# Kernel tuning notes

Hardware: AMD Instinct MI355X
Metric: run time of the kernel (lower is better)

Reference implementation:

```python
import jax, jax.numpy as jnp
import numpy as np

DIM = 1024      # dim
FW = 14         # focal_window
FL = 2          # focal_level
FF = 4          # focal_factor


def _dwconv_gelu(x, w, b):
    # x: [B, C, S], w: [C, 1, k] depthwise kernel, torch 'same' padding
    k = w.shape[-1]
    y = jax.lax.conv_general_dilated(
        x, w, window_strides=(1,), padding=[((k - 1) // 2, k // 2)],
        feature_group_count=x.shape[1], dimension_numbers=('NCH', 'OIH', 'NCH'))
    return jax.nn.gelu(y + b[None, :, None], approximate=False)


def setup_inputs() -> dict:
    key = jax.random.key(0)
    ks = jax.random.split(key, 8)
    B, S, D = 8, 4096, DIM
    P = 2 * D + FL + 1  # 2051
    s = 0.02
    return {
        'input': jax.random.normal(ks[0], (B, S, D), jnp.float32),
        'W_in': jax.random.normal(ks[1], (D, P), jnp.float32) * s,
        'b_in': jnp.zeros((P,), jnp.float32),
        'w0': jax.random.normal(ks[2], (D, 1, FW), jnp.float32) * s,
        'b0': jnp.zeros((D,), jnp.float32),
        'w1': jax.random.normal(ks[3], (D, 1, FF + FW), jnp.float32) * s,  # kernel 18
        'b1': jnp.zeros((D,), jnp.float32),
        'W_ctx': jax.random.normal(ks[4], (D, D), jnp.float32) * s,
        'b_ctx': jnp.zeros((D,), jnp.float32),
        'W_out': jax.random.normal(ks[5], (D, D), jnp.float32) * s,
        'b_out': jnp.zeros((D,), jnp.float32),
    }


def reference(input, W_in, b_in, w0, b0, w1, b1, W_ctx, b_ctx, W_out, b_out):
    D = DIM
    # in_proj then permute to channel-first [B, 2D+FL+1, S]
    proj = (input @ W_in + b_in).transpose(0, 2, 1)
    query = proj[:, :D]            # [B, D, S]
    ctx = proj[:, D:2 * D]         # [B, D, S]
    gates = proj[:, 2 * D:]        # [B, FL+1, S]
    # hierarchical depthwise conv pyramid (context fed through successive levels)
    c0 = _dwconv_gelu(ctx, w0, b0)
    c1 = _dwconv_gelu(c0, w1, b1)
    context_all = c0 * gates[:, 0:1] + c1 * gates[:, 1:2]
    # global context branch
    g = jax.nn.gelu(c1.mean(axis=-1), approximate=False)  # [B, D]
    context_all = context_all + g[..., None] * gates[:, FL:FL + 1]
    # context_proj is a 1x1 conv == per-position linear over channels
    modulator = jnp.einsum('oc,bcs->bos', W_ctx, context_all) + b_ctx[None, :, None]
    out = (query * modulator).transpose(0, 2, 1)  # [B, S, D]
    return out @ W_out + b_out
```

## Files before the change

### kernel.cpp

```cpp
#include <hip/hip_runtime.h>

#define DIMC 1024
#define BATCH 8
#define SEQ 4096
#define BS (BATCH*SEQ)
#define PCOL 2051

typedef unsigned short ushort_t;
typedef __attribute__((ext_vector_type(8))) short short8;
typedef __attribute__((ext_vector_type(4))) float f32x4;
typedef __attribute__((ext_vector_type(4))) unsigned short us4;

__device__ __forceinline__ float bf2f(ushort_t u) {
    union { unsigned u32; float f; } v; v.u32 = ((unsigned)u) << 16; return v.f;
}
__device__ __forceinline__ ushort_t f2bf(float f) {
    union { float f; unsigned u; } v; v.f = f;
    unsigned r = v.u + 0x7fffu + ((v.u >> 16) & 1u);
    return (ushort_t)(r >> 16);
}
__device__ __forceinline__ float gelu_exact(float x) {
    return 0.5f * x * (1.0f + erff(x * 0.7071067811865475f));
}
__device__ __forceinline__ void gld16(const ushort_t* g, ushort_t* l) {
    __builtin_amdgcn_global_load_lds(
        (const __attribute__((address_space(1))) unsigned int*)g,
        (__attribute__((address_space(3))) unsigned int*)l, 16, 0, 0);
}

__global__ void cvt_f32_bf16(const float* __restrict__ src, ushort_t* __restrict__ dst, int n) {
    int i = (blockIdx.x * 256 + threadIdx.x) * 4;
    if (i >= n) return;
    f32x4 v = *(const f32x4*)(src + i);
    us4 o;
    #pragma unroll
    for (int j = 0; j < 4; j++) o[j] = f2bf(v[j]);
    *(us4*)(dst + i) = o;
}

__global__ void transpose_cvt(const float* __restrict__ src, ushort_t* __restrict__ dst,
                              int ld, int K) {
    __shared__ float tile[32][33];
    int tx = threadIdx.x & 31, ty = threadIdx.x >> 5;
    int n0 = blockIdx.x * 32, k0 = blockIdx.y * 32;
    #pragma unroll
    for (int j = 0; j < 4; j++)
        tile[ty + j * 8][tx] = src[(size_t)(k0 + ty + j * 8) * ld + n0 + tx];
    __syncthreads();
    #pragma unroll
    for (int j = 0; j < 4; j++)
        dst[(size_t)(n0 + ty + j * 8) * K + k0 + tx] = f2bf(tile[tx][ty + j * 8]);
}

__global__ void pack_gatesw(const float* __restrict__ W_in, float* __restrict__ wg) {
    int d = blockIdx.x * 256 + threadIdx.x;
    if (d >= 1024) return;
    const float* p = W_in + (size_t)d * PCOL + 2048;
    wg[d] = p[0]; wg[1024 + d] = p[1]; wg[2048 + d] = p[2];
}

__global__ void cvt_gates(const float* __restrict__ input, const float* __restrict__ wg,
                          const float* __restrict__ b_in, ushort_t* __restrict__ ibf,
                          float* __restrict__ gates) {
    int row = blockIdx.x, tid = threadIdx.x;
    int lane = tid & 63, wave = tid >> 6;
    size_t base = (size_t)row * 1024 + tid * 4;
    f32x4 v = *(const f32x4*)(input + base);
    us4 o;
    #pragma unroll
    for (int j = 0; j < 4; j++) o[j] = f2bf(v[j]);
    *(us4*)(ibf + base) = o;
    f32x4 w0v = *(const f32x4*)(wg + tid * 4);
    f32x4 w1v = *(const f32x4*)(wg + 1024 + tid * 4);
    f32x4 w2v = *(const f32x4*)(wg + 2048 + tid * 4);
    float a0 = 0, a1 = 0, a2 = 0;
    #pragma unroll
    for (int j = 0; j < 4; j++) { a0 += v[j] * w0v[j]; a1 += v[j] * w1v[j]; a2 += v[j] * w2v[j]; }
    #pragma unroll
    for (int off = 32; off; off >>= 1) {
        a0 += __shfl_down(a0, off, 64);
        a1 += __shfl_down(a1, off, 64);
        a2 += __shfl_down(a2, off, 64);
    }
    __shared__ float red[4][3];
    if (lane == 0) { red[wave][0] = a0; red[wave][1] = a1; red[wave][2] = a2; }
    __syncthreads();
    if (tid == 0) {
        gates[row * 4 + 0] = red[0][0] + red[1][0] + red[2][0] + red[3][0] + b_in[2048];
        gates[row * 4 + 1] = red[0][1] + red[1][1] + red[2][1] + red[3][1] + b_in[2049];
        gates[row * 4 + 2] = red[0][2] + red[1][2] + red[2][2] + red[3][2] + b_in[2050];
    }
}

template<int FUSEQ, int F32OUT>
__global__ __launch_bounds__(256, 2)
void gemm_bt(const ushort_t* __restrict__ A, const ushort_t* __restrict__ Bt,
             const float* __restrict__ bias, void* __restrict__ C,
             const ushort_t* __restrict__ Q, int K, int ldc, int ldq) {
    __shared__ ushort_t lA[128 * 32];
    __shared__ ushort_t lB[128 * 32];
    const int tid = threadIdx.x, lane = tid & 63, wave = tid >> 6;
    const int bn = blockIdx.x, bm = blockIdx.y;
    const int wm = (wave >> 1) * 64, wn = (wave & 1) * 64;
    const int lr = lane & 15, kq = (lane >> 4) * 8;

    const ushort_t* Ag = A + (size_t)bm * 128 * K;
    const ushort_t* Bg = Bt + (size_t)bn * 128 * K;

    f32x4 acc[4][4];
    #pragma unroll
    for (int i = 0; i < 4; i++)
        #pragma unroll
        for (int j = 0; j < 4; j++)
            #pragma unroll
            for (int r = 0; r < 4; r++) acc[i][j][r] = 0.0f;

    for (int k0 = 0; k0 < K; k0 += 32) {
        #pragma unroll
        for (int i = 0; i < 2; i++) {
            int cb = i * 256 + wave * 64;
            int c  = cb + lane;
            int row = c >> 2, kk = (c & 3) << 3;
            gld16(Ag + (size_t)row * K + kk, &lA[cb << 3]);
            gld16(Bg + (size_t)row * K + kk, &lB[cb << 3]);
        }
        Ag += 32; Bg += 32;
        __syncthreads();

        short8 af[4], bfr[4];
        #pragma unroll
        for (int mt = 0; mt < 4; mt++)
            af[mt] = *(const short8*)&lA[(wm + mt * 16 + lr) * 32 + kq];
        #pragma unroll
        for (int nt = 0; nt < 4; nt++)
            bfr[nt] = *(const short8*)&lB[(wn + nt * 16 + lr) * 32 + kq];
        #pragma unroll
        for (int mt = 0; mt < 4; mt++)
            #pragma unroll
            for (int nt = 0; nt < 4; nt++)
                acc[mt][nt] = __builtin_amdgcn_mfma_f32_16x16x32_bf16(
                    af[mt], bfr[nt], acc[mt][nt], 0, 0, 0);
        __syncthreads();
    }

    const int lq = lane >> 4;
    #pragma unroll
    for (int mt = 0; mt < 4; mt++) {
        #pragma unroll
        for (int r = 0; r < 4; r++) {
            int row = bm * 128 + wm + mt * 16 + lq * 4 + r;
            size_t rowc = (size_t)row * ldc;
            #pragma unroll
            for (int nt = 0; nt < 4; nt++) {
                int col = bn * 128 + wn + nt * 16 + lr;
                float v = acc[mt][nt][r] + bias[col];
                if (FUSEQ) v *= bf2f(Q[(size_t)row * ldq + col]);
                if (F32OUT) ((float*)C)[rowc + col] = v;
                else        ((ushort_t*)C)[rowc + col] = f2bf(v);
            }
        }
    }
}

template<int KW, int PADL, int DOMEAN>
__global__ __launch_bounds__(256)
void dwconv_gelu2(const ushort_t* __restrict__ X, int ldx, int x0,
                  const float* __restrict__ W, const float* __restrict__ Bv,
                  ushort_t* __restrict__ Y, float* __restrict__ G) {
    const int R = 64 + KW - 1;
    __shared__ float xs[(64 + KW - 1) * 64];
    int tid = threadIdx.x;
    int s0 = blockIdx.x * 64, d0 = blockIdx.y * 64, b = blockIdx.z;
    for (int c = tid; c < R * 8; c += 256) {
        int r = c >> 3, dd = (c & 7) * 8;
        int s = s0 + r - PADL;
        float f[8];
        if (s >= 0 && s < SEQ) {
            short8 u = *(const short8*)&X[(size_t)(b * SEQ + s) * ldx + x0 + d0 + dd];
            #pragma unroll
            for (int j = 0; j < 8; j++) f[j] = bf2f((ushort_t)u[j]);
        } else {
            #pragma unroll
            for (int j = 0; j < 8; j++) f[j] = 0.f;
        }
        f32x4 v0 = {f[0], f[1], f[2], f[3]}, v1 = {f[4], f[5], f[6], f[7]};
        *(f32x4*)&xs[r * 64 + dd] = v0;
        *(f32x4*)&xs[r * 64 + dd + 4] = v1;
    }
    int d = tid & 63, sc = tid >> 6;
    float wr[KW];
    #pragma unroll
    for (int t = 0; t < KW; t++) wr[t] = W[(size_t)(d0 + d) * KW + t];
    float bb = Bv[d0 + d];
    __syncthreads();
    float xw[16 + KW - 1];
    #pragma unroll
    for (int r = 0; r < 16 + KW - 1; r++) xw[r] = xs[(sc * 16 + r) * 64 + d];
    float psum = 0.f;
    #pragma unroll
    for (int i = 0; i < 16; i++) {
        float acc = bb;
        #pragma unroll
        for (int t = 0; t < KW; t++) acc += wr[t] * xw[i + t];
        float gv = gelu_exact(acc);
        if (DOMEAN) psum += gv;
        Y[(size_t)(b * SEQ + s0 + sc * 16 + i) * 1024 + d0 + d] = f2bf(gv);
    }
    if (DOMEAN) {
        __shared__ float rs[256];
        rs[tid] = psum;
        __syncthreads();
        if (sc == 0)
            atomicAdd(&G[b * 1024 + d0 + d], rs[d] + rs[64 + d] + rs[128 + d] + rs[192 + d]);
    }
}

__global__ void gelu_g(const float* __restrict__ G, float* __restrict__ gG) {
    int i = blockIdx.x * 256 + threadIdx.x;
    if (i < BATCH * 1024) gG[i] = gelu_exact(G[i] * (1.0f / (float)SEQ));
}

__global__ void combine2(const ushort_t* __restrict__ C0, const ushort_t* __restrict__ C1,
                         const float* __restrict__ gates, const float* __restrict__ gG,
                         ushort_t* __restrict__ CA) {
    int row = blockIdx.x * 2 + (threadIdx.x >> 7);
    int c = (threadIdx.x & 127) * 8;
    int b = row >> 12;
    float g0 = gates[row * 4 + 0], g1 = gates[row * 4 + 1], g2 = gates[row * 4 + 2];
    size_t base = (size_t)row * 1024 + c;
    short8 u0 = *(const short8*)&C0[base];
    short8 u1 = *(const short8*)&C1[base];
    f32x4 gv0 = *(const f32x4*)&gG[b * 1024 + c];
    f32x4 gv1 = *(const f32x4*)&gG[b * 1024 + c + 4];
    short8 o;
    #pragma unroll
    for (int j = 0; j < 8; j++) {
        float gg = (j < 4) ? gv0[j] : gv1[j - 4];
        float v = bf2f((ushort_t)u0[j]) * g0 + bf2f((ushort_t)u1[j]) * g1 + gg * g2;
        o[j] = (short)f2bf(v);
    }
    *(short8*)&CA[base] = o;
}

extern "C" void kernel_launch(void* const* d_in, const int* in_sizes, int n_in,
                              void* d_out, int out_size, void* d_ws, size_t ws_size,
                              hipStream_t stream) {
    const float* input = (const float*)d_in[0];
    const float* W_in  = (const float*)d_in[1];
    const float* b_in  = (const float*)d_in[2];
    const float* w0    = (const float*)d_in[3];
    const float* b0    = (const float*)d_in[4];
    const float* w1    = (const float*)d_in[5];
    const float* b1    = (const float*)d_in[6];
    const float* W_ctx = (const float*)d_in[7];
    const float* b_ctx = (const float*)d_in[8];
    const float* W_out = (const float*)d_in[9];
    const float* b_out = (const float*)d_in[10];

    char* ws = (char*)d_ws;
    size_t o = 0;
    ushort_t* ibf   = (ushort_t*)(ws + o); o += (size_t)BS * 1024 * 2;
    ushort_t* proj  = (ushort_t*)(ws + o); o += (size_t)BS * 2048 * 2;
    ushort_t* c0    = (ushort_t*)(ws + o); o += (size_t)BS * 1024 * 2;
    ushort_t* c1    = (ushort_t*)(ws + o); o += (size_t)BS * 1024 * 2;
    float*    gates = (float*)   (ws + o); o += (size_t)BS * 4 * 4;
    float*    G     = (float*)   (ws + o); o += (size_t)BATCH * 1024 * 4;
    float*    gG    = (float*)   (ws + o); o += (size_t)BATCH * 1024 * 4;
    float*    wg    = (float*)   (ws + o); o += (size_t)3 * 1024 * 4;
    ushort_t* winT  = (ushort_t*)(ws + o); o += (size_t)2048 * 1024 * 2;
    ushort_t* wctxB = (ushort_t*)(ws + o); o += (size_t)1024 * 1024 * 2;
    ushort_t* woutT = (ushort_t*)(ws + o); o += (size_t)1024 * 1024 * 2;
    ushort_t* ca = ibf;
    ushort_t* Y  = c0;

    hipMemsetAsync(G, 0, BATCH * 1024 * sizeof(float), stream);
    pack_gatesw<<<4, 256, 0, stream>>>(W_in, wg);
    transpose_cvt<<<dim3(2048 / 32, 1024 / 32), 256, 0, stream>>>(W_in, winT, PCOL, 1024);
    cvt_f32_bf16<<<1024 * 1024 / 4 / 256, 256, 0, stream>>>(W_ctx, wctxB, 1024 * 1024);
    transpose_cvt<<<dim3(1024 / 32, 1024 / 32), 256, 0, stream>>>(W_out, woutT, 1024, 1024);
    cvt_gates<<<BS, 256, 0, stream>>>(input, wg, b_in, ibf, gates);
    gemm_bt<0, 0><<<dim3(16, 256), 256, 0, stream>>>(ibf, winT, b_in, proj, nullptr, 1024, 2048, 0);
    dwconv_gelu2<14, 6, 0><<<dim3(SEQ / 64, 16, BATCH), 256, 0, stream>>>(proj, 2048, 1024, w0, b0, c0, nullptr);
    dwconv_gelu2<18, 8, 1><<<dim3(SEQ / 64, 16, BATCH), 256, 0, stream>>>(c0, 1024, 0, w1, b1, c1, G);
    gelu_g<<<BATCH * 1024 / 256, 256, 0, stream>>>(G, gG);
    combine2<<<BS / 2, 256, 0, stream>>>(c0, c1, gates, gG, ca);
    gemm_bt<1, 0><<<dim3(8, 256), 256, 0, stream>>>(ca, wctxB, b_ctx, Y, proj, 1024, 1024, 2048);
    gemm_bt<0, 1><<<dim3(8, 256), 256, 0, stream>>>(Y, woutT, b_out, d_out, nullptr, 1024, 1024, 0);
}
```

Baseline: 760.5 us.

## Fuse both depthwise convs with gating and fold global context into GEMM epilogue

```diff
diff --git a/kernel.cpp b/kernel.cpp
--- a/kernel.cpp
+++ b/kernel.cpp
@@ -92,11 +92,12 @@
     }
 }
 
-template<int FUSEQ, int F32OUT>
+template<int MODE>
 __global__ __launch_bounds__(256, 2)
 void gemm_bt(const ushort_t* __restrict__ A, const ushort_t* __restrict__ Bt,
              const float* __restrict__ bias, void* __restrict__ C,
-             const ushort_t* __restrict__ Q, int K, int ldc, int ldq) {
+             const ushort_t* __restrict__ Q, const float* __restrict__ gates,
+             const float* __restrict__ vb, int K, int ldc, int ldq) {
     __shared__ ushort_t lA[128 * 32];
     __shared__ ushort_t lB[128 * 32];
     const int tid = threadIdx.x, lane = tid & 63, wave = tid >> 6;
@@ -144,39 +145,48 @@
     }
 
     const int lq = lane >> 4;
+    const int bbatch = (bm * 128) >> 12;
     #pragma unroll
     for (int mt = 0; mt < 4; mt++) {
         #pragma unroll
         for (int r = 0; r < 4; r++) {
             int row = bm * 128 + wm + mt * 16 + lq * 4 + r;
             size_t rowc = (size_t)row * ldc;
+            float g2;
+            if (MODE == 1) g2 = gates[row * 4 + 2];
             #pragma unroll
             for (int nt = 0; nt < 4; nt++) {
                 int col = bn * 128 + wn + nt * 16 + lr;
                 float v = acc[mt][nt][r] + bias[col];
-                if (FUSEQ) v *= bf2f(Q[(size_t)row * ldq + col]);
-                if (F32OUT) ((float*)C)[rowc + col] = v;
-                else        ((ushort_t*)C)[rowc + col] = f2bf(v);
+                if (MODE == 1) {
+                    v += g2 * vb[bbatch * 1024 + col];
+                    v *= bf2f(Q[(size_t)row * ldq + col]);
+                }
+                if (MODE == 2) ((float*)C)[rowc + col] = v;
+                else           ((ushort_t*)C)[rowc + col] = f2bf(v);
             }
         }
     }
 }
 
-template<int KW, int PADL, int DOMEAN>
 __global__ __launch_bounds__(256)
-void dwconv_gelu2(const ushort_t* __restrict__ X, int ldx, int x0,
-                  const float* __restrict__ W, const float* __restrict__ Bv,
-                  ushort_t* __restrict__ Y, float* __restrict__ G) {
-    const int R = 64 + KW - 1;
-    __shared__ float xs[(64 + KW - 1) * 64];
-    int tid = threadIdx.x;
-    int s0 = blockIdx.x * 64, d0 = blockIdx.y * 64, b = blockIdx.z;
-    for (int c = tid; c < R * 8; c += 256) {
+void dwconv_fused(const ushort_t* __restrict__ proj,
+                  const float* __restrict__ w0, const float* __restrict__ b0,
+                  const float* __restrict__ w1, const float* __restrict__ b1,
+                  const float* __restrict__ gates,
+                  ushort_t* __restrict__ P, float* __restrict__ G) {
+    __shared__ float xc[94 * 64];
+    __shared__ float x0[81 * 64];
+    __shared__ float gl[2][64];
+    __shared__ float rs[256];
+    const int tid = threadIdx.x;
+    const int s0 = blockIdx.x * 64, d0 = blockIdx.y * 64, b = blockIdx.z;
+    for (int c = tid; c < 94 * 8; c += 256) {
         int r = c >> 3, dd = (c & 7) * 8;
-        int s = s0 + r - PADL;
+        int s = s0 - 14 + r;
         float f[8];
         if (s >= 0 && s < SEQ) {
-            short8 u = *(const short8*)&X[(size_t)(b * SEQ + s) * ldx + x0 + d0 + dd];
+            short8 u = *(const short8*)&proj[(size_t)(b * SEQ + s) * 2048 + 1024 + d0 + dd];
             #pragma unroll
             for (int j = 0; j < 8; j++) f[j] = bf2f((ushort_t)u[j]);
         } else {
@@ -184,62 +194,76 @@
             for (int j = 0; j < 8; j++) f[j] = 0.f;
         }
         f32x4 v0 = {f[0], f[1], f[2], f[3]}, v1 = {f[4], f[5], f[6], f[7]};
-        *(f32x4*)&xs[r * 64 + dd] = v0;
-        *(f32x4*)&xs[r * 64 + dd + 4] = v1;
-    }
-    int d = tid & 63, sc = tid >> 6;
-    float wr[KW];
-    #pragma unroll
-    for (int t = 0; t < KW; t++) wr[t] = W[(size_t)(d0 + d) * KW + t];
-    float bb = Bv[d0 + d];
-    __syncthreads();
-    float xw[16 + KW - 1];
-    #pragma unroll
-    for (int r = 0; r < 16 + KW - 1; r++) xw[r] = xs[(sc * 16 + r) * 64 + d];
+        *(f32x4*)&xc[r * 64 + dd] = v0;
+        *(f32x4*)&xc[r * 64 + dd + 4] = v1;
+    }
+    if (tid < 64) gl[0][tid] = gates[(size_t)(b * SEQ + s0 + tid) * 4 + 0];
+    else if (tid < 128) gl[1][tid - 64] = gates[(size_t)(b * SEQ + s0 + tid - 64) * 4 + 1];
+    const int d = tid & 63, sc = tid >> 6;
+    float wr0[14], wr1[18];
+    #pragma unroll
+    for (int t = 0; t < 14; t++) wr0[t] = w0[(size_t)(d0 + d) * 14 + t];
+    float bb0 = b0[d0 + d];
+    #pragma unroll
+    for (int t = 0; t < 18; t++) wr1[t] = w1[(size_t)(d0 + d) * 18 + t];
+    float bb1 = b1[d0 + d];
+    __syncthreads();
+    {
+        float xw[34];
+        int r0 = sc * 20;
+        #pragma unroll
+        for (int r = 0; r < 34; r++) xw[r] = xc[(r0 + r) * 64 + d];
+        #pragma unroll
+        for (int i = 0; i < 21; i++) {
+            int rr = r0 + i;
+            int s = s0 - 8 + rr;
+            float acc = bb0;
+            #pragma unroll
+            for (int t = 0; t < 14; t++) acc += wr0[t] * xw[i + t];
+            x0[rr * 64 + d] = (s >= 0 && s < SEQ) ? gelu_exact(acc) : 0.f;
+        }
+    }
+    __syncthreads();
+    float xw1[33];
+    #pragma unroll
+    for (int r = 0; r < 33; r++) xw1[r] = x0[(sc * 16 + r) * 64 + d];
     float psum = 0.f;
     #pragma unroll
     for (int i = 0; i < 16; i++) {
-        float acc = bb;
-        #pragma unroll
-        for (int t = 0; t < KW; t++) acc += wr[t] * xw[i + t];
-        float gv = gelu_exact(acc);
-        if (DOMEAN) psum += gv;
-        Y[(size_t)(b * SEQ + s0 + sc * 16 + i) * 1024 + d0 + d] = f2bf(gv);
-    }
-    if (DOMEAN) {
-        __shared__ float rs[256];
-        rs[tid] = psum;
-        __syncthreads();
-        if (sc == 0)
-            atomicAdd(&G[b * 1024 + d0 + d], rs[d] + rs[64 + d] + rs[128 + d] + rs[192 + d]);
-    }
-}
-
-__global__ void gelu_g(const float* __restrict__ G, float* __restrict__ gG) {
-    int i = blockIdx.x * 256 + threadIdx.x;
-    if (i < BATCH * 1024) gG[i] = gelu_exact(G[i] * (1.0f / (float)SEQ));
-}
-
-__global__ void combine2(const ushort_t* __restrict__ C0, const ushort_t* __restrict__ C1,
-                         const float* __restrict__ gates, const float* __restrict__ gG,
-                         ushort_t* __restrict__ CA) {
-    int row = blockIdx.x * 2 + (threadIdx.x >> 7);
-    int c = (threadIdx.x & 127) * 8;
-    int b = row >> 12;
-    float g0 = gates[row * 4 + 0], g1 = gates[row * 4 + 1], g2 = gates[row * 4 + 2];
-    size_t base = (size_t)row * 1024 + c;
-    short8 u0 = *(const short8*)&C0[base];
-    short8 u1 = *(const short8*)&C1[base];
-    f32x4 gv0 = *(const f32x4*)&gG[b * 1024 + c];
-    f32x4 gv1 = *(const f32x4*)&gG[b * 1024 + c + 4];
-    short8 o;
-    #pragma unroll
-    for (int j = 0; j < 8; j++) {
-        float gg = (j < 4) ? gv0[j] : gv1[j - 4];
-        float v = bf2f((ushort_t)u0[j]) * g0 + bf2f((ushort_t)u1[j]) * g1 + gg * g2;
-        o[j] = (short)f2bf(v);
-    }
-    *(short8*)&CA[base] = o;
+        float acc = bb1;
+        #pragma unroll
+        for (int t = 0; t < 18; t++) acc += wr1[t] * xw1[i + t];
+        float c1 = gelu_exact(acc);
+        psum += c1;
+        float c0v = xw1[i + 8];
+        int sl = sc * 16 + i;
+        float pv = c0v * gl[0][sl] + c1 * gl[1][sl];
+        P[(size_t)(b * SEQ + s0 + sl) * 1024 + d0 + d] = f2bf(pv);
+    }
+    rs[tid] = psum;
+    __syncthreads();
+    if (sc == 0)
+        atomicAdd(&G[b * 1024 + d0 + d], rs[d] + rs[64 + d] + rs[128 + d] + rs[192 + d]);
+}
+
+__global__ __launch_bounds__(256)
+void gemv_v(const float* __restrict__ G, const ushort_t* __restrict__ wctxB,
+            float* __restrict__ v) {
+    __shared__ float gg[1024];
+    const int tid = threadIdx.x, b = blockIdx.y;
+    for (int i = tid; i < 1024; i += 256)
+        gg[i] = gelu_exact(G[b * 1024 + i] * (1.0f / (float)SEQ));
+    __syncthreads();
+    const int w = tid >> 6, lane = tid & 63;
+    const int o = blockIdx.x * 4 + w;
+    const ushort_t* wr = wctxB + (size_t)o * 1024;
+    float acc = 0.f;
+    #pragma unroll
+    for (int j = 0; j < 16; j++)
+        acc += gg[j * 64 + lane] * bf2f(wr[j * 64 + lane]);
+    #pragma unroll
+    for (int off = 32; off; off >>= 1) acc += __shfl_down(acc, off, 64);
+    if (lane == 0) v[b * 1024 + o] = acc;
 }
 
 extern "C" void kernel_launch(void* const* d_in, const int* in_sizes, int n_in,
@@ -261,17 +285,15 @@
     size_t o = 0;
     ushort_t* ibf   = (ushort_t*)(ws + o); o += (size_t)BS * 1024 * 2;
     ushort_t* proj  = (ushort_t*)(ws + o); o += (size_t)BS * 2048 * 2;
-    ushort_t* c0    = (ushort_t*)(ws + o); o += (size_t)BS * 1024 * 2;
-    ushort_t* c1    = (ushort_t*)(ws + o); o += (size_t)BS * 1024 * 2;
+    ushort_t* Y     = (ushort_t*)(ws + o); o += (size_t)BS * 1024 * 2;
     float*    gates = (float*)   (ws + o); o += (size_t)BS * 4 * 4;
     float*    G     = (float*)   (ws + o); o += (size_t)BATCH * 1024 * 4;
-    float*    gG    = (float*)   (ws + o); o += (size_t)BATCH * 1024 * 4;
+    float*    v     = (float*)   (ws + o); o += (size_t)BATCH * 1024 * 4;
     float*    wg    = (float*)   (ws + o); o += (size_t)3 * 1024 * 4;
     ushort_t* winT  = (ushort_t*)(ws + o); o += (size_t)2048 * 1024 * 2;
     ushort_t* wctxB = (ushort_t*)(ws + o); o += (size_t)1024 * 1024 * 2;
     ushort_t* woutT = (ushort_t*)(ws + o); o += (size_t)1024 * 1024 * 2;
-    ushort_t* ca = ibf;
-    ushort_t* Y  = c0;
+    ushort_t* P = ibf;
 
     hipMemsetAsync(G, 0, BATCH * 1024 * sizeof(float), stream);
     pack_gatesw<<<4, 256, 0, stream>>>(W_in, wg);
@@ -279,11 +301,9 @@
     cvt_f32_bf16<<<1024 * 1024 / 4 / 256, 256, 0, stream>>>(W_ctx, wctxB, 1024 * 1024);
     transpose_cvt<<<dim3(1024 / 32, 1024 / 32), 256, 0, stream>>>(W_out, woutT, 1024, 1024);
     cvt_gates<<<BS, 256, 0, stream>>>(input, wg, b_in, ibf, gates);
-    gemm_bt<0, 0><<<dim3(16, 256), 256, 0, stream>>>(ibf, winT, b_in, proj, nullptr, 1024, 2048, 0);
-    dwconv_gelu2<14, 6, 0><<<dim3(SEQ / 64, 16, BATCH), 256, 0, stream>>>(proj, 2048, 1024, w0, b0, c0, nullptr);
-    dwconv_gelu2<18, 8, 1><<<dim3(SEQ / 64, 16, BATCH), 256, 0, stream>>>(c0, 1024, 0, w1, b1, c1, G);
-    gelu_g<<<BATCH * 1024 / 256, 256, 0, stream>>>(G, gG);
-    combine2<<<BS / 2, 256, 0, stream>>>(c0, c1, gates, gG, ca);
-    gemm_bt<1, 0><<<dim3(8, 256), 256, 0, stream>>>(ca, wctxB, b_ctx, Y, proj, 1024, 1024, 2048);
-    gemm_bt<0, 1><<<dim3(8, 256), 256, 0, stream>>>(Y, woutT, b_out, d_out, nullptr, 1024, 1024, 0);
-}
+    gemm_bt<0><<<dim3(16, 256), 256, 0, stream>>>(ibf, winT, b_in, proj, nullptr, nullptr, nullptr, 1024, 2048, 0);
+    dwconv_fused<<<dim3(SEQ / 64, 16, BATCH), 256, 0, stream>>>(proj, w0, b0, w1, b1, gates, P, G);
+    gemv_v<<<dim3(256, BATCH), 256, 0, stream>>>(G, wctxB, v);
+    gemm_bt<1><<<dim3(8, 256), 256, 0, stream>>>(P, wctxB, b_ctx, Y, proj, gates, v, 1024, 1024, 2048);
+    gemm_bt<2><<<dim3(8, 256), 256, 0, stream>>>(Y, woutT, b_out, d_out, nullptr, nullptr, nullptr, 1024, 1024, 0);
+}
```

Result: faster. 735.9 us (-3.2%).
